# Kernel optimization log

Hardware: AMD Instinct MI355X
Metric: run time of the kernel (lower is better)

The kernel has to match this reference:

```python
import jax, jax.numpy as jnp
import numpy as np

B, N = 4, 512
C_IN, RES, SR = 256, 7, 2
FC_DIM = 1024
NUM_CLASSES, BOX_DIM, BINS = 3, 6, 12
OUT_CH = NUM_CLASSES * (1 + BOX_DIM + 2 * BINS) + 1  # 94
IMG = 512
STRIDES = (8, 16, 32)


def setup_inputs() -> dict:
    key = jax.random.key(0)
    ks = jax.random.split(key, 12)
    feat_p3 = jax.random.normal(ks[0], (B, C_IN, IMG // 8, IMG // 8), jnp.float32)
    feat_p4 = jax.random.normal(ks[1], (B, C_IN, IMG // 16, IMG // 16), jnp.float32)
    feat_p5 = jax.random.normal(ks[2], (B, C_IN, IMG // 32, IMG // 32), jnp.float32)
    cy = jax.random.uniform(ks[3], (B, N), minval=64.0, maxval=448.0)
    cx = jax.random.uniform(ks[4], (B, N), minval=64.0, maxval=448.0)
    h = jax.random.uniform(ks[5], (B, N), minval=16.0, maxval=120.0)
    w = jax.random.uniform(ks[6], (B, N), minval=16.0, maxval=120.0)
    bbox2d = jnp.stack([cy - h / 2, cx - w / 2, cy + h / 2, cx + w / 2], -1)  # tlbr
    anchors = jnp.stack([cy, cx, h, w], -1)  # (y, x, l, w)
    anchor_id = jax.random.randint(ks[7], (B, N), 0, 9, dtype=jnp.int32)
    flat = C_IN * RES * RES
    fc1_w = jax.random.normal(ks[8], (FC_DIM, flat), jnp.float32) * 0.01
    fc1_b = jnp.zeros((FC_DIM,), jnp.float32)
    bn1_g = jnp.ones((FC_DIM,), jnp.float32)
    bn1_b = jnp.zeros((FC_DIM,), jnp.float32)
    fc2_w = jax.random.normal(ks[9], (FC_DIM, FC_DIM), jnp.float32) * 0.02
    fc2_b = jnp.zeros((FC_DIM,), jnp.float32)
    bn2_g = jnp.ones((FC_DIM,), jnp.float32)
    bn2_b = jnp.zeros((FC_DIM,), jnp.float32)
    pred_w = jax.random.normal(ks[10], (OUT_CH, FC_DIM), jnp.float32) * 0.02
    pred_b = jnp.zeros((OUT_CH,), jnp.float32)
    return dict(feat_p3=feat_p3, feat_p4=feat_p4, feat_p5=feat_p5, bbox2d=bbox2d,
                anchors=anchors, anchor_id=anchor_id, fc1_w=fc1_w, fc1_b=fc1_b,
                bn1_g=bn1_g, bn1_b=bn1_b, fc2_w=fc2_w, fc2_b=fc2_b,
                bn2_g=bn2_g, bn2_b=bn2_b, pred_w=pred_w, pred_b=pred_b)


def _roi_align(feat, boxes, scale):
    # feat: [C,H,W]; boxes: [N,4] tlbr in image coords; aligned=True ROIAlign.
    C, H, W = feat.shape
    S = RES * SR
    t = boxes[:, 0] * scale - 0.5
    l = boxes[:, 1] * scale - 0.5
    bh = (boxes[:, 2] - boxes[:, 0]) * scale / RES  # bin height
    bw = (boxes[:, 3] - boxes[:, 1]) * scale / RES
    g = (jnp.arange(S, dtype=feat.dtype) + 0.5) / SR  # sample offsets in bin units
    ys = t[:, None] + g[None, :] * bh[:, None]  # [N,S]
    xs = l[:, None] + g[None, :] * bw[:, None]
    yc = jnp.clip(ys, 0.0, H - 1.0)
    xc = jnp.clip(xs, 0.0, W - 1.0)
    y0 = jnp.floor(yc)
    x0 = jnp.floor(xc)
    y0i = y0.astype(jnp.int32)
    x0i = x0.astype(jnp.int32)
    y1i = jnp.minimum(y0i + 1, H - 1)
    x1i = jnp.minimum(x0i + 1, W - 1)
    ly = yc - y0
    lx = xc - x0

    def gat(yi, xi):  # -> [C,N,S,S]
        return feat[:, yi[:, :, None], xi[:, None, :]]

    w00 = ((1 - ly)[:, :, None] * (1 - lx)[:, None, :])[None]
    w01 = ((1 - ly)[:, :, None] * lx[:, None, :])[None]
    w10 = (ly[:, :, None] * (1 - lx)[:, None, :])[None]
    w11 = (ly[:, :, None] * lx[:, None, :])[None]
    v = gat(y0i, x0i) * w00 + gat(y0i, x1i) * w01 + gat(y1i, x0i) * w10 + gat(y1i, x1i) * w11
    v = jnp.transpose(v, (1, 0, 2, 3)).reshape(-1, C, RES, SR, RES, SR)
    return v.mean((3, 5))  # [N,C,RES,RES] avg over sampling grid


def _bn_train(x, g, b):
    m = x.mean(0)
    v = x.var(0)
    return (x - m) * jax.lax.rsqrt(v + 1e-5) * g + b


def _forward(feat_p3, feat_p4, feat_p5, bbox2d, anchors, fc1_w, fc1_b, bn1_g, bn1_b,
             fc2_w, fc2_b, bn2_g, bn2_b, pred_w, pred_b, anchor_id):
    feats = (feat_p3, feat_p4, feat_p5)
    lvl = anchor_id // 3  # [B,N] feature-level assignment
    # box_pooler: pool every box at every level, then select its assigned level
    # (equivalent to the torch gather/sort/cat dispatch, in original box order).
    sel = 0.0
    for i, s in enumerate(STRIDES):
        pooled = jax.vmap(lambda f, bx, sc=1.0 / s: _roi_align(f, bx, sc))(feats[i], bbox2d)
        sel = sel + pooled * (lvl == i)[..., None, None, None].astype(pooled.dtype)
    x = sel.reshape(B * N, -1)  # [B*N, C*7*7]
    x = jax.nn.relu(_bn_train(x @ fc1_w.T + fc1_b, bn1_g, bn1_b))
    x = jax.nn.relu(_bn_train(x @ fc2_w.T + fc2_b, bn2_g, bn2_b))
    pred = (x @ pred_w.T + pred_b).reshape(B, N, OUT_CH)
    # decode: slice per-loss channels then apply box deltas per category
    c0 = NUM_CLASSES + 1
    cat = pred[..., :c0]  # [B,N,4]
    b1 = c0 + NUM_CLASSES * BOX_DIM
    bbox3d = pred[..., c0:b1].reshape(B, N, NUM_CLASSES, BOX_DIM)
    yaw_cls = pred[..., b1:b1 + NUM_CLASSES * BINS]
    yaw_res = pred[..., b1 + NUM_CLASSES * BINS:]
    delta = bbox3d[..., :4]  # yxlw deltas per category
    zh = bbox3d[..., 4:]
    stride_px = jnp.exp2(lvl.astype(pred.dtype) + 3.0)  # 8/16/32
    yx = anchors[:, :, None, :2] + delta[..., :2] * stride_px[..., None, None]
    lw = anchors[:, :, None, 2:] * jnp.exp(jnp.clip(delta[..., 2:], -4.0, 4.0))
    box_out = jnp.concatenate([yx, lw, zh], -1).reshape(B, N, NUM_CLASSES * BOX_DIM)
    return jnp.concatenate([cat, box_out, yaw_cls, yaw_res], -1)  # [B,N,94]


def reference(feat_p3, feat_p4, feat_p5, bbox2d, anchors, anchor_id, fc1_w, fc1_b,
              bn1_g, bn1_b, fc2_w, fc2_b, bn2_g, bn2_b, pred_w, pred_b):
    return _forward(feat_p3, feat_p4, feat_p5, bbox2d, anchors, fc1_w, fc1_b, bn1_g,
                    bn1_b, fc2_w, fc2_b, bn2_g, bn2_b, pred_w, pred_b, anchor_id)
```

## Files before the change

kernel.cpp:

```cpp
#include <hip/hip_runtime.h>
#include <hip/hip_bf16.h>

typedef __attribute__((ext_vector_type(8))) short short8;
typedef __attribute__((ext_vector_type(4))) float floatx4;
typedef __attribute__((ext_vector_type(4))) unsigned short ushort4v;

#define DEVI __device__ __forceinline__


DEVI unsigned short f2bf(float v) {
  union { __hip_bfloat16 h; unsigned short u; } cv;
  cv.h = __float2bfloat16(v);
  return cv.u;
}
DEVI short f2bfs(float v) { return (short)f2bf(v); }

DEVI void gload16(const void* gptr, void* lptr) {
  __builtin_amdgcn_global_load_lds(
      (const __attribute__((address_space(1))) unsigned int*)gptr,
      (__attribute__((address_space(3))) unsigned int*)(unsigned long long)(uintptr_t)lptr,
      16, 0, 0);
}

__global__ void cvt_bf16x4_kernel(const float4* __restrict__ src,
                                  ushort4v* __restrict__ dst, size_t n4) {
  size_t i = (size_t)blockIdx.x * blockDim.x + threadIdx.x;
  if (i >= n4) return;
  float4 v = src[i];
  ushort4v o;
  o[0] = f2bf(v.x); o[1] = f2bf(v.y); o[2] = f2bf(v.z); o[3] = f2bf(v.w);
  dst[i] = o;
}

__global__ void cvt_pad_pred_kernel(const float* __restrict__ src,
                                    unsigned short* __restrict__ dst) {
  int i = blockIdx.x * blockDim.x + threadIdx.x;
  if (i >= 96 * 1024) return;
  int row = i >> 10;
  dst[i] = (row < 94) ? f2bf(src[i]) : (unsigned short)0;
}

__global__ __launch_bounds__(256) void roi_mm6_kernel(
    const float* __restrict__ p3, const float* __restrict__ p4,
    const float* __restrict__ p5, const float* __restrict__ bbox,
    const int* __restrict__ aid, unsigned short* __restrict__ X) {
  constexpr int PS = 260;
  constexpr int PBS = 280;
  __shared__ float Pf[32 * PS];
  __shared__ float wyx[238];
  __shared__ int sy0[14], sx0[14];
  __shared__ float sly[14], slx[14];
  unsigned short* Pb = (unsigned short*)Pf;

  const int box = blockIdx.x;
  const int oct = blockIdx.y;
  const int b = box >> 9;
  const int tid = threadIdx.x;
  const int lane = tid & 63, wid = tid >> 6;

  const int lvl = aid[box] / 3;
  const int H = 64 >> lvl;
  const int HH = H * H;
  const float* base = (lvl == 0) ? p3 : ((lvl == 1) ? p4 : p5);
  const float scale = 0.125f / (float)(1 << lvl);

  if (tid < 28) {
    int s = tid;
    bool isY = s < 14;
    int k = isY ? s : s - 14;
    float lo = bbox[box * 4 + (isY ? 0 : 1)];
    float hi = bbox[box * 4 + (isY ? 2 : 3)];
    float t = lo * scale - 0.5f;
    float cell = (hi - lo) * scale * (1.0f / 7.0f);
    float pos = t + ((float)k + 0.5f) * 0.5f * cell;
    pos = fminf(fmaxf(pos, 0.0f), (float)(H - 1));
    int i0 = (int)floorf(pos);
    if (i0 > H - 2) i0 = H - 2;
    float fr = pos - (float)i0;
    if (isY) { sy0[k] = i0; sly[k] = fr; }
    else     { sx0[k] = i0; slx[k] = fr; }
  }
  __syncthreads();

  const int ryb = min(sy0[0], H - 16);
  const int rxb = min(sx0[0], H - 16);
  const float* fb = base + ((size_t)b * 256 + oct * 32) * HH + ryb * H + rxb;

  if (tid < 224) {
    int j = tid;
    bool isY = j < 112;
    int k2 = isY ? j : j - 112;
    int py = k2 >> 4, r = k2 & 15;
    int o0 = isY ? ryb : rxb;
    float acc = 0.f;
#pragma unroll
    for (int ss = 0; ss < 2; ++ss) {
      int s = 2 * py + ss;
      int rel = (isY ? sy0[s] : sx0[s]) - o0;
      float fr = isY ? sly[s] : slx[s];
      if (r == rel)     acc += 1.0f - fr;
      if (r == rel + 1) acc += fr;
    }
    wyx[(isY ? 0 : 119) + py * 17 + r] = acc * 0.5f;
  }

  {
    const int r = lane >> 2, c4 = (lane & 3) * 4;
    const float* src0 = fb + r * H + c4;
#pragma unroll
    for (int it = 0; it < 8; ++it) {
      int ch = it * 4 + wid;
      gload16(src0 + (size_t)ch * HH, &Pf[ch * PS] + lane * 4);
    }
  }
  __syncthreads();

  {
    const int cch = tid & 31, rp = tid >> 5;
    const float* src = &Pf[cch * PS + rp * 32];
    floatx4 v[8];
#pragma unroll
    for (int m = 0; m < 8; ++m) v[m] = *(const floatx4*)(src + 4 * m);
    __syncthreads();
    unsigned int d[16];
#pragma unroll
    for (int m = 0; m < 8; ++m) {
      d[2 * m]     = (unsigned int)f2bf(v[m][0]) | ((unsigned int)f2bf(v[m][1]) << 16);
      d[2 * m + 1] = (unsigned int)f2bf(v[m][2]) | ((unsigned int)f2bf(v[m][3]) << 16);
    }
    unsigned short* dst = &Pb[cch * PBS + rp * 32];
#pragma unroll
    for (int m = 0; m < 4; ++m)
      *(uint4*)(dst + m * 8) = make_uint4(d[4 * m], d[4 * m + 1], d[4 * m + 2], d[4 * m + 3]);
  }

  const int fr = lane & 15, fg = lane >> 4;
  const int cell = wid * 16 + fr;
  const int py = (cell * 37) >> 8;
  const int px = cell - py * 7;
  float xv[8], wyv[8];
  {
    const float* xp = &wyx[119 + px * 17 + (fg & 1) * 8];
#pragma unroll
    for (int e = 0; e < 8; ++e) xv[e] = xp[e];
    const float* wp = &wyx[py * 17 + (fg >> 1)];
#pragma unroll
    for (int kk = 0; kk < 8; ++kk) wyv[kk] = wp[2 * kk];
  }
  __syncthreads();

  floatx4 acc0 = (floatx4){0.f, 0.f, 0.f, 0.f};
  floatx4 acc1 = (floatx4){0.f, 0.f, 0.f, 0.f};

#pragma unroll
  for (int kk = 0; kk < 8; ++kk) {
    short8 af0 = *(const short8*)&Pb[fr * PBS + kk * 32 + fg * 8];
    short8 af1 = *(const short8*)&Pb[(16 + fr) * PBS + kk * 32 + fg * 8];
    short8 bfr;
    const float w = wyv[kk];
#pragma unroll
    for (int e = 0; e < 8; ++e) bfr[e] = f2bfs(w * xv[e]);
    acc0 = __builtin_amdgcn_mfma_f32_16x16x32_bf16(af0, bfr, acc0, 0, 0, 0);
    acc1 = __builtin_amdgcn_mfma_f32_16x16x32_bf16(af1, bfr, acc1, 0, 0, 0);
  }

  if (cell < 49) {
    unsigned short* xb = X + (size_t)box * 12544 + (size_t)(oct * 32) * 49 + cell;
#pragma unroll
    for (int q = 0; q < 4; ++q) {
      xb[(fg * 4 + q) * 49] = f2bf(acc0[q]);
      xb[(16 + fg * 4 + q) * 49] = f2bf(acc1[q]);
    }
  }
}

template <int KSPLIT>
__global__ __launch_bounds__(256) void gemm_bt_swz(
    const unsigned short* __restrict__ A, const unsigned short* __restrict__ Bw,
    float* __restrict__ C, int M, int N, int K) {
  constexpr int BM = 128, BN = 128, BK = 64;
  __shared__ unsigned short As[BM * BK];
  __shared__ unsigned short Bs[BN * BK];

  const int tid = threadIdx.x;
  const int lane = tid & 63, wid = tid >> 6;
  const int wr = wid >> 1, wc = wid & 1;
  const int tm = blockIdx.x * BM, tn = blockIdx.y * BN;
  const int fr = lane & 15, fg = lane >> 4;

  const int kLen = K / KSPLIT;
  const int kTiles = kLen / BK;
  const int kBeg = blockIdx.z * kLen;
  float* Cz = C + (size_t)blockIdx.z * M * N;

  floatx4 acc[4][4];
#pragma unroll
  for (int i = 0; i < 4; ++i)
#pragma unroll
    for (int j = 0; j < 4; ++j)
      acc[i][j] = (floatx4){0.f, 0.f, 0.f, 0.f};

  for (int t = 0; t < kTiles; ++t) {
    const int k0 = kBeg + t * BK;
#pragma unroll
    for (int s = tid; s < BM * 8; s += 256) {
      int row = s >> 3, sl = s & 7;
      int slg = sl ^ (row & 7);
      gload16(&A[(size_t)(tm + row) * K + k0 + slg * 8], &As[s * 8]);
    }
#pragma unroll
    for (int s = tid; s < BN * 8; s += 256) {
      int row = s >> 3, sl = s & 7;
      int slg = sl ^ (row & 7);
      gload16(&Bw[(size_t)(tn + row) * K + k0 + slg * 8], &Bs[s * 8]);
    }
    __syncthreads();

#pragma unroll
    for (int kk = 0; kk < 2; ++kk) {
      short8 af[4], bf[4];
#pragma unroll
      for (int i = 0; i < 4; ++i) {
        int row = wr * 64 + i * 16 + fr;
        int sl = (kk * 4 + fg) ^ (row & 7);
        af[i] = *reinterpret_cast<const short8*>(&As[(row * 8 + sl) * 8]);
      }
#pragma unroll
      for (int j = 0; j < 4; ++j) {
        int row = wc * 64 + j * 16 + fr;
        int sl = (kk * 4 + fg) ^ (row & 7);
        bf[j] = *reinterpret_cast<const short8*>(&Bs[(row * 8 + sl) * 8]);
      }
#pragma unroll
      for (int i = 0; i < 4; ++i)
#pragma unroll
        for (int j = 0; j < 4; ++j)
          acc[i][j] = __builtin_amdgcn_mfma_f32_16x16x32_bf16(af[i], bf[j], acc[i][j], 0, 0, 0);
    }
    __syncthreads();
  }

#pragma unroll
  for (int i = 0; i < 4; ++i)
#pragma unroll
    for (int j = 0; j < 4; ++j)
#pragma unroll
      for (int q = 0; q < 4; ++q) {
        int rr = tm + wr * 64 + i * 16 + fg * 4 + q;
        int cc = tn + wc * 64 + j * 16 + fr;
        Cz[(size_t)rr * N + cc] = acc[i][j][q];
      }
}

template <int BM, int BN, int WAVES_M, int WAVES_N, int KSPLIT>
__global__ __launch_bounds__(256) void gemm_bt_kernel(
    const unsigned short* __restrict__ A, const unsigned short* __restrict__ Bw,
    float* __restrict__ C, int M, int N, int K) {
  constexpr int BK = 32;
  constexpr int WM = BM / WAVES_M, WN = BN / WAVES_N;
  constexpr int AF = WM / 16, BF = WN / 16;
  constexpr int ASLOT = BM * 4;
  constexpr int BSLOT = BN * 4;
  __shared__ unsigned short As[BM * BK];
  __shared__ unsigned short Bs[BN * BK];

  const int tid = threadIdx.x;
  const int lane = tid & 63, wid = tid >> 6;
  const int wr = wid / WAVES_N, wc = wid % WAVES_N;
  const int tm = blockIdx.x * BM, tn = blockIdx.y * BN;
  const int fr = lane & 15, fg = lane >> 4;

  const int kLen = K / KSPLIT;
  const int kBeg = blockIdx.z * kLen;
  float* Cz = C + (size_t)blockIdx.z * M * N;

  floatx4 acc[AF][BF];
#pragma unroll
  for (int i = 0; i < AF; ++i)
#pragma unroll
    for (int j = 0; j < BF; ++j)
      acc[i][j] = (floatx4){0.f, 0.f, 0.f, 0.f};

  for (int k0 = kBeg; k0 < kBeg + kLen; k0 += BK) {
#pragma unroll
    for (int s = tid; s < ASLOT; s += 256) {
      int row = s >> 2, kb = (s & 3) << 3;
      gload16(&A[(size_t)(tm + row) * K + k0 + kb], &As[s * 8]);
    }
#pragma unroll
    for (int s = tid; s < BSLOT; s += 256) {
      int row = s >> 2, kb = (s & 3) << 3;
      gload16(&Bw[(size_t)(tn + row) * K + k0 + kb], &Bs[s * 8]);
    }
    __syncthreads();

    short8 af[AF], bfv[BF];
#pragma unroll
    for (int i = 0; i < AF; ++i)
      af[i] = *reinterpret_cast<const short8*>(&As[(wr * WM + i * 16 + fr) * BK + fg * 8]);
#pragma unroll
    for (int j = 0; j < BF; ++j)
      bfv[j] = *reinterpret_cast<const short8*>(&Bs[(wc * WN + j * 16 + fr) * BK + fg * 8]);
#pragma unroll
    for (int i = 0; i < AF; ++i)
#pragma unroll
      for (int j = 0; j < BF; ++j)
        acc[i][j] = __builtin_amdgcn_mfma_f32_16x16x32_bf16(af[i], bfv[j], acc[i][j], 0, 0, 0);
    __syncthreads();
  }

#pragma unroll
  for (int i = 0; i < AF; ++i)
#pragma unroll
    for (int j = 0; j < BF; ++j)
#pragma unroll
      for (int q = 0; q < 4; ++q) {
        int rr = tm + wr * WM + i * 16 + fg * 4 + q;
        int cc = tn + wc * WN + j * 16 + fr;
        Cz[(size_t)rr * N + cc] = acc[i][j][q];
      }
}

__global__ void bn_stats_red_kernel(const float* __restrict__ Yp, float* __restrict__ Yred,
                                    float* __restrict__ psum, float* __restrict__ psq,
                                    int Ncols, int rowsPer, int P, size_t pstride) {
  int c = blockIdx.x * blockDim.x + threadIdx.x;
  int r0 = blockIdx.y * rowsPer;
  float s = 0.f, ss = 0.f;
  for (int r = 0; r < rowsPer; ++r) {
    size_t idx = (size_t)(r0 + r) * Ncols + c;
    float v = Yp[idx];
    for (int p = 1; p < P; ++p) v += Yp[idx + (size_t)p * pstride];
    Yred[idx] = v;
    s += v;
    ss += v * v;
  }
  psum[(size_t)blockIdx.y * Ncols + c] = s;
  psq[(size_t)blockIdx.y * Ncols + c] = ss;
}

__global__ void bn_finalize_kernel(const float* __restrict__ psum, const float* __restrict__ psq,
                                   const float* __restrict__ g, const float* __restrict__ b,
                                   float* __restrict__ scale, float* __restrict__ shift,
                                   int Ncols, int P, float invM) {
  int c = blockIdx.x * blockDim.x + threadIdx.x;
  if (c >= Ncols) return;
  float s = 0.f, ss = 0.f;
  for (int p = 0; p < P; ++p) {
    s += psum[(size_t)p * Ncols + c];
    ss += psq[(size_t)p * Ncols + c];
  }
  float mean = s * invM;
  float var = ss * invM - mean * mean;
  float rstd = rsqrtf(var + 1e-5f);
  float sc = rstd * g[c];
  scale[c] = sc;
  shift[c] = b[c] - mean * sc;
}

__global__ void bn_apply4_kernel(const float4* __restrict__ Y, const float* __restrict__ scale,
                                 const float* __restrict__ shift, ushort4v* __restrict__ X,
                                 int colGroupsMask, int total4) {
  int i = blockIdx.x * blockDim.x + threadIdx.x;
  if (i >= total4) return;
  int c0 = (i & colGroupsMask) * 4;
  float4 v = Y[i];
  ushort4v o;
  o[0] = f2bf(fmaxf(v.x * scale[c0 + 0] + shift[c0 + 0], 0.0f));
  o[1] = f2bf(fmaxf(v.y * scale[c0 + 1] + shift[c0 + 1], 0.0f));
  o[2] = f2bf(fmaxf(v.z * scale[c0 + 2] + shift[c0 + 2], 0.0f));
  o[3] = f2bf(fmaxf(v.w * scale[c0 + 3] + shift[c0 + 3], 0.0f));
  X[i] = o;
}

__global__ void decode_kernel(const float* __restrict__ Y3, const float* __restrict__ pb,
                              const float* __restrict__ anchors, const int* __restrict__ aid,
                              float* __restrict__ out) {
  int i = blockIdx.x * blockDim.x + threadIdx.x;
  if (i >= 2048 * 94) return;
  int bn = i / 94;
  int ch = i - bn * 94;
  size_t idx = (size_t)bn * 96 + ch;
  float v = Y3[idx] + Y3[idx + 2048 * 96] + Y3[idx + 2 * 2048 * 96] + Y3[idx + 3 * 2048 * 96];
  v += pb[ch];
  float o = v;
  if (ch >= 4 && ch < 22) {
    int q = ch - 4;
    int d = q % 6;
    if (d < 2) {
      float stride_px = (float)(8 << (aid[bn] / 3));
      o = anchors[(size_t)bn * 4 + d] + v * stride_px;
    } else if (d < 4) {
      float cl = fminf(fmaxf(v, -4.0f), 4.0f);
      o = anchors[(size_t)bn * 4 + d] * expf(cl);
    }
  }
  out[i] = o;
}

extern "C" void kernel_launch(void* const* d_in, const int* in_sizes, int n_in,
                              void* d_out, int out_size, void* d_ws, size_t ws_size,
                              hipStream_t stream) {
  const float* feat_p3   = (const float*)d_in[0];
  const float* feat_p4   = (const float*)d_in[1];
  const float* feat_p5   = (const float*)d_in[2];
  const float* bbox2d    = (const float*)d_in[3];
  const float* anchors   = (const float*)d_in[4];
  const int*   anchor_id = (const int*)d_in[5];
  const float* fc1_w     = (const float*)d_in[6];
  const float* bn1_g     = (const float*)d_in[8];
  const float* bn1_b     = (const float*)d_in[9];
  const float* fc2_w     = (const float*)d_in[10];
  const float* bn2_g     = (const float*)d_in[12];
  const float* bn2_b     = (const float*)d_in[13];
  const float* pred_w    = (const float*)d_in[14];
  const float* pred_b    = (const float*)d_in[15];
  float* out = (float*)d_out;

  const int M = 2048;
  const int K1 = 12544;
  const int FC = 1024;
  const int RG = 128;

  char* ws = (char*)d_ws;
  auto alloc = [&](size_t bytes) -> char* {
    char* p = ws;
    ws += (bytes + 255) & ~(size_t)255;
    return p;
  };
  unsigned short* W1b  = (unsigned short*)alloc((size_t)FC * K1 * 2);
  unsigned short* W2b  = (unsigned short*)alloc((size_t)FC * FC * 2);
  unsigned short* W3b  = (unsigned short*)alloc((size_t)96 * FC * 2);
  unsigned short* X1   = (unsigned short*)alloc((size_t)M * K1 * 2);
  float*          Yp   = (float*)alloc((size_t)4 * M * FC * 4);
  float*          Yr   = (float*)alloc((size_t)M * FC * 4);
  unsigned short* X2   = (unsigned short*)alloc((size_t)M * FC * 2);
  unsigned short* X3   = (unsigned short*)alloc((size_t)M * FC * 2);
  float*          Y3   = (float*)alloc((size_t)4 * M * 96 * 4);
  float*          ps   = (float*)alloc((size_t)RG * FC * 4);
  float*          pq   = (float*)alloc((size_t)RG * FC * 4);
  float*          sc1  = (float*)alloc((size_t)FC * 4);
  float*          sh1  = (float*)alloc((size_t)FC * 4);
  float*          sc2  = (float*)alloc((size_t)FC * 4);
  float*          sh2  = (float*)alloc((size_t)FC * 4);

  {
    size_t n4 = (size_t)FC * K1 / 4;
    cvt_bf16x4_kernel<<<(unsigned)((n4 + 255) / 256), 256, 0, stream>>>(
        (const float4*)fc1_w, (ushort4v*)W1b, n4);
  }
  {
    size_t n4 = (size_t)FC * FC / 4;
    cvt_bf16x4_kernel<<<(unsigned)((n4 + 255) / 256), 256, 0, stream>>>(
        (const float4*)fc2_w, (ushort4v*)W2b, n4);
  }
  cvt_pad_pred_kernel<<<(96 * 1024) / 256, 256, 0, stream>>>(pred_w, W3b);

  roi_mm6_kernel<<<dim3(2048, 8), 256, 0, stream>>>(feat_p3, feat_p4, feat_p5,
                                                    bbox2d, anchor_id, X1);

  gemm_bt_swz<4><<<dim3(M / 128, FC / 128, 4), 256, 0, stream>>>(X1, W1b, Yp, M, FC, K1);

  bn_stats_red_kernel<<<dim3(FC / 256, RG), 256, 0, stream>>>(Yp, Yr, ps, pq, FC, M / RG, 4, (size_t)M * FC);
  bn_finalize_kernel<<<FC / 256, 256, 0, stream>>>(ps, pq, bn1_g, bn1_b, sc1, sh1, FC, RG, 1.0f / M);
  bn_apply4_kernel<<<(M * FC / 4) / 256, 256, 0, stream>>>(
      (const float4*)Yr, sc1, sh1, (ushort4v*)X2, FC / 4 - 1, M * FC / 4);

  gemm_bt_swz<2><<<dim3(M / 128, FC / 128, 2), 256, 0, stream>>>(X2, W2b, Yp, M, FC, FC);

  bn_stats_red_kernel<<<dim3(FC / 256, RG), 256, 0, stream>>>(Yp, Yr, ps, pq, FC, M / RG, 2, (size_t)M * FC);
  bn_finalize_kernel<<<FC / 256, 256, 0, stream>>>(ps, pq, bn2_g, bn2_b, sc2, sh2, FC, RG, 1.0f / M);
  bn_apply4_kernel<<<(M * FC / 4) / 256, 256, 0, stream>>>(
      (const float4*)Yr, sc2, sh2, (ushort4v*)X3, FC / 4 - 1, M * FC / 4);

  gemm_bt_kernel<64, 96, 2, 2, 4><<<dim3(M / 64, 1, 4), 256, 0, stream>>>(X3, W3b, Y3, M, 96, FC);

  decode_kernel<<<(2048 * 94 + 255) / 256, 256, 0, stream>>>(Y3, pred_b, anchors, anchor_id, out);
}
```

Measured before the change: 257.0 us.

## Merge weight conversions into ROI kernel and add XCD-aware GEMM block swizzle

Folds the three weight fp32-to-bf16 conversion kernels into the ROI-align launch as extra blocks, so four launches become one and the memory-bound conversions can overlap the ROI work. Separately, it remaps GEMM workgroup IDs so that consecutive logical tiles land on the same XCD, aiming for better L2 reuse of A/B tiles on the multi-die MI355X. The fused kernel's shared-memory footprint now applies to the conversion blocks too, which may limit their occupancy.

```diff
diff --git a/kernel.cpp b/kernel.cpp
--- a/kernel.cpp
+++ b/kernel.cpp
@@ -22,40 +22,53 @@
       16, 0, 0);
 }
 
-__global__ void cvt_bf16x4_kernel(const float4* __restrict__ src,
-                                  ushort4v* __restrict__ dst, size_t n4) {
-  size_t i = (size_t)blockIdx.x * blockDim.x + threadIdx.x;
-  if (i >= n4) return;
-  float4 v = src[i];
-  ushort4v o;
-  o[0] = f2bf(v.x); o[1] = f2bf(v.y); o[2] = f2bf(v.z); o[3] = f2bf(v.w);
-  dst[i] = o;
-}
-
-__global__ void cvt_pad_pred_kernel(const float* __restrict__ src,
-                                    unsigned short* __restrict__ dst) {
-  int i = blockIdx.x * blockDim.x + threadIdx.x;
-  if (i >= 96 * 1024) return;
-  int row = i >> 10;
-  dst[i] = (row < 94) ? f2bf(src[i]) : (unsigned short)0;
-}
-
-__global__ __launch_bounds__(256) void roi_mm6_kernel(
+#define ROI_BLKS   16384
+#define CVT1_END   28928
+#define CVT2_END   29952
+#define GRID_TOTAL 30336
+
+__global__ __launch_bounds__(256) void prep_roi_kernel(
     const float* __restrict__ p3, const float* __restrict__ p4,
     const float* __restrict__ p5, const float* __restrict__ bbox,
-    const int* __restrict__ aid, unsigned short* __restrict__ X) {
+    const int* __restrict__ aid, unsigned short* __restrict__ X,
+    const float* __restrict__ fc1_w, unsigned short* __restrict__ W1b,
+    const float* __restrict__ fc2_w, unsigned short* __restrict__ W2b,
+    const float* __restrict__ pred_w, unsigned short* __restrict__ W3b) {
   constexpr int PS = 260;
   constexpr int PBS = 280;
   __shared__ float Pf[32 * PS];
   __shared__ float wyx[238];
   __shared__ int sy0[14], sx0[14];
   __shared__ float sly[14], slx[14];
+
+  const int bid = blockIdx.x;
+  const int tid = threadIdx.x;
+
+  if (bid >= ROI_BLKS) {
+    if (bid < CVT1_END) {
+      size_t i = (size_t)(bid - ROI_BLKS) * 256 + tid;
+      float4 v = ((const float4*)fc1_w)[i];
+      ushort4v o;
+      o[0] = f2bf(v.x); o[1] = f2bf(v.y); o[2] = f2bf(v.z); o[3] = f2bf(v.w);
+      ((ushort4v*)W1b)[i] = o;
+    } else if (bid < CVT2_END) {
+      size_t i = (size_t)(bid - CVT1_END) * 256 + tid;
+      float4 v = ((const float4*)fc2_w)[i];
+      ushort4v o;
+      o[0] = f2bf(v.x); o[1] = f2bf(v.y); o[2] = f2bf(v.z); o[3] = f2bf(v.w);
+      ((ushort4v*)W2b)[i] = o;
+    } else {
+      int i = (bid - CVT2_END) * 256 + tid;
+      int row = i >> 10;
+      W3b[i] = (row < 94) ? f2bf(pred_w[i]) : (unsigned short)0;
+    }
+    return;
+  }
+
   unsigned short* Pb = (unsigned short*)Pf;
-
-  const int box = blockIdx.x;
-  const int oct = blockIdx.y;
+  const int box = bid & 2047;
+  const int oct = bid >> 11;
   const int b = box >> 9;
-  const int tid = threadIdx.x;
   const int lane = tid & 63, wid = tid >> 6;
 
   const int lvl = aid[box] / 3;
@@ -185,13 +198,27 @@
   const int tid = threadIdx.x;
   const int lane = tid & 63, wid = tid >> 6;
   const int wr = wid >> 1, wc = wid & 1;
-  const int tm = blockIdx.x * BM, tn = blockIdx.y * BN;
   const int fr = lane & 15, fg = lane >> 4;
+
+  int bx = blockIdx.x, by = blockIdx.y, bz = blockIdx.z;
+  {
+    const int gx = gridDim.x, gy = gridDim.y;
+    const int nwg = gx * gy * gridDim.z;
+    if ((nwg & 7) == 0) {
+      int lin = bx + gx * (by + gy * bz);
+      int swz = (lin & 7) * (nwg >> 3) + (lin >> 3);
+      bx = swz % gx;
+      int t = swz / gx;
+      by = t % gy;
+      bz = t / gy;
+    }
+  }
+  const int tm = bx * BM, tn = by * BN;
 
   const int kLen = K / KSPLIT;
   const int kTiles = kLen / BK;
-  const int kBeg = blockIdx.z * kLen;
-  float* Cz = C + (size_t)blockIdx.z * M * N;
+  const int kBeg = bz * kLen;
+  float* Cz = C + (size_t)bz * M * N;
 
   floatx4 acc[4][4];
 #pragma unroll
@@ -444,20 +471,9 @@
   float*          sc2  = (float*)alloc((size_t)FC * 4);
   float*          sh2  = (float*)alloc((size_t)FC * 4);
 
-  {
-    size_t n4 = (size_t)FC * K1 / 4;
-    cvt_bf16x4_kernel<<<(unsigned)((n4 + 255) / 256), 256, 0, stream>>>(
-        (const float4*)fc1_w, (ushort4v*)W1b, n4);
-  }
-  {
-    size_t n4 = (size_t)FC * FC / 4;
-    cvt_bf16x4_kernel<<<(unsigned)((n4 + 255) / 256), 256, 0, stream>>>(
-        (const float4*)fc2_w, (ushort4v*)W2b, n4);
-  }
-  cvt_pad_pred_kernel<<<(96 * 1024) / 256, 256, 0, stream>>>(pred_w, W3b);
-
-  roi_mm6_kernel<<<dim3(2048, 8), 256, 0, stream>>>(feat_p3, feat_p4, feat_p5,
-                                                    bbox2d, anchor_id, X1);
+  prep_roi_kernel<<<GRID_TOTAL, 256, 0, stream>>>(
+      feat_p3, feat_p4, feat_p5, bbox2d, anchor_id, X1,
+      fc1_w, W1b, fc2_w, W2b, pred_w, W3b);
 
   gemm_bt_swz<4><<<dim3(M / 128, FC / 128, 4), 256, 0, stream>>>(X1, W1b, Yp, M, FC, K1);
 
```

Measured after the change: 251.1 us. -2.3%, faster.
